# Optimization experiments

Hardware: AMD Instinct MI355X
Metric: run time of the kernel (lower is better)

The kernel has to match this reference:

```python
import jax, jax.numpy as jnp
import numpy as np

N = 100000
E = 3200000
IN_DIM, HID_DIM, OUT_DIM = 29, 64, 2


def setup_inputs() -> dict:
    key = jax.random.key(0)
    k1, k2, k3, k4, k5 = jax.random.split(key, 5)
    x = jax.random.normal(k1, (N, IN_DIM), dtype=jnp.float32)
    edge_index = jax.random.randint(k2, (2, E), 0, N, dtype=jnp.int64)
    # GCNConv params: glorot-ish weights, zero bias (bias added after aggregation)
    W1 = jax.random.normal(k3, (IN_DIM, HID_DIM), dtype=jnp.float32) * (1.0 / np.sqrt(IN_DIM))
    b1 = jnp.zeros((HID_DIM,), dtype=jnp.float32)
    W2 = jax.random.normal(k4, (HID_DIM, OUT_DIM), dtype=jnp.float32) * (1.0 / np.sqrt(HID_DIM))
    b2 = jnp.zeros((OUT_DIM,), dtype=jnp.float32)
    return {"x": x, "edge_index": edge_index, "W1": W1, "b1": b1, "W2": W2, "b2": b2}


def _gcn_norm(edge_index, n_nodes):
    # PyG gcn_norm with add_self_loops=True, symmetric D^-1/2 A D^-1/2
    loop = jnp.arange(n_nodes, dtype=edge_index.dtype)
    src = jnp.concatenate([edge_index[0], loop])
    dst = jnp.concatenate([edge_index[1], loop])
    deg = jax.ops.segment_sum(jnp.ones_like(dst, dtype=jnp.float32), dst, num_segments=n_nodes)
    dinv = jnp.where(deg > 0, jax.lax.rsqrt(deg), 0.0)
    norm = dinv[src] * dinv[dst]  # [E + N]
    return src, dst, norm


def _gcn_conv(x, src, dst, norm, W, b):
    h = x @ W                      # [N, d_out] -- transform first (smaller msgs)
    msg = h[src] * norm[:, None]   # [E+N, d_out] gather + scale
    out = jax.ops.segment_sum(msg, dst, num_segments=x.shape[0])  # scatter-add
    return out + b


def reference(x, edge_index, W1, b1, W2, b2):
    src, dst, norm = _gcn_norm(edge_index, x.shape[0])
    h = _gcn_conv(x, src, dst, norm, W1, b1)
    h = jax.nn.relu(h)
    out = _gcn_conv(h, src, dst, norm, W2, b2)
    return out
```

## Files before the change

### kernel.cpp

```cpp
#include <hip/hip_runtime.h>

#define N_NODES 100000
#define N_EDGES 3200000
#define IN_DIM  29
#define HID_DIM 64
#define NBUCK   391
#define BNODES  256
#define CAP     10496
#define PEPT    16
#define PEPB    16384
#define PSTAGE  22272

#define OFF_CUR   0
#define OFF_ROWS  512
#define OFF_ROWE  100512
#define OFF_DINV  200512
#define OFF_ZS    300512
#define OFF_EBUF  500544
#define OFF_XS    4604480

static __device__ __forceinline__ unsigned short f2bf(float f) {
    unsigned u = __float_as_uint(f);
    u += 0x7fffu + ((u >> 16) & 1u);
    return (unsigned short)(u >> 16);
}

static __device__ __forceinline__ void unpack_add(float4& acc, uint2 a) {
    acc.x += __uint_as_float(a.x << 16);
    acc.y += __uint_as_float(a.x & 0xFFFF0000u);
    acc.z += __uint_as_float(a.y << 16);
    acc.w += __uint_as_float(a.y & 0xFFFF0000u);
}

__global__ __launch_bounds__(1024) void partition_kernel(const int* __restrict__ ei,
        int* __restrict__ gcursor, int* __restrict__ ebuf) {
    __shared__ int lhist[NBUCK];
    __shared__ int lcur[NBUCK];
    __shared__ int gbase[NBUCK];
    __shared__ int soff[NBUCK];
    __shared__ int sc[NBUCK];
    __shared__ int stage[PSTAGE];
    int tid = threadIdx.x;
    for (int i = tid; i < NBUCK; i += 1024) lhist[i] = 0;
    __syncthreads();

    int base = blockIdx.x * PEPB + tid * PEPT;
    bool valid = (base < N_EDGES);
    if (valid) {
        const int4* dp = (const int4*)(ei + N_EDGES + base);
        #pragma unroll
        for (int q = 0; q < 4; ++q) {
            int4 t = dp[q];
            atomicAdd(&lhist[t.x >> 8], 1); atomicAdd(&lhist[t.y >> 8], 1);
            atomicAdd(&lhist[t.z >> 8], 1); atomicAdd(&lhist[t.w >> 8], 1);
        }
    }
    __syncthreads();
    int c = 0, p = 0;
    if (tid < NBUCK) { c = lhist[tid]; p = (c + 15) & ~15; sc[tid] = p; }
    __syncthreads();
    for (int off = 1; off < NBUCK; off <<= 1) {
        int t = 0;
        if (tid < NBUCK && tid >= off) t = sc[tid - off];
        __syncthreads();
        if (tid < NBUCK) sc[tid] += t;
        __syncthreads();
    }
    if (tid < NBUCK) {
        int so = sc[tid] - p;
        soff[tid] = so;
        lcur[tid] = so;
        gbase[tid] = p ? (tid * CAP + atomicAdd(&gcursor[tid], p)) : 0;
    }
    __syncthreads();
    if (valid) {
        const int4* dp = (const int4*)(ei + N_EDGES + base);
        const int4* sp = (const int4*)(ei + base);
        #pragma unroll
        for (int q = 0; q < 4; ++q) {
            int4 d = dp[q];
            int4 s = sp[q];
            int pos;
            pos = atomicAdd(&lcur[d.x >> 8], 1); stage[pos] = s.x | ((d.x & 255) << 17);
            pos = atomicAdd(&lcur[d.y >> 8], 1); stage[pos] = s.y | ((d.y & 255) << 17);
            pos = atomicAdd(&lcur[d.z >> 8], 1); stage[pos] = s.z | ((d.z & 255) << 17);
            pos = atomicAdd(&lcur[d.w >> 8], 1); stage[pos] = s.w | ((d.w & 255) << 17);
        }
    }
    __syncthreads();
    if (tid < NBUCK) {
        int endReal = lcur[tid];
        int endPad  = soff[tid] + (((lhist[tid]) + 15) & ~15);
        for (int k = endReal; k < endPad; ++k) stage[k] = -1;
    }
    __syncthreads();
    int wv = tid >> 6, ln = tid & 63;
    for (int b = wv; b < NBUCK; b += 16) {
        int np = (lhist[b] + 15) & ~15;
        int so = soff[b], gb = gbase[b];
        for (int k = ln; k < np; k += 64)
            ebuf[gb + k] = stage[so + k];
    }
}

__global__ __launch_bounds__(1024) void bucketsort_kernel(const int* __restrict__ gcursor,
        int* __restrict__ ebuf, int* __restrict__ rowStart, int* __restrict__ rowEnd,
        float* __restrict__ dinv, const float* __restrict__ x,
        unsigned int* __restrict__ xsb, float* __restrict__ zs) {
    __shared__ int   cnt[BNODES];
    __shared__ int   cur[BNODES];
    __shared__ float dls[BNODES];
    __shared__ int   stage[CAP];
    __shared__ int   szp_sh;
    int b = blockIdx.x, tid = threadIdx.x;
    if (tid < BNODES) cnt[tid] = 0;
    __syncthreads();
    int base = b * CAP;
    int size = gcursor[b];

    for (int j = tid; j < size; j += 1024) {
        unsigned p = (unsigned)ebuf[base + j];
        if (p != 0xFFFFFFFFu) atomicAdd(&cnt[p >> 17], 1);
    }
    __syncthreads();

    int v = 0, vp = 0;
    if (tid < BNODES) { v = cnt[tid]; vp = (v + 7) & ~7; cur[tid] = vp; }
    __syncthreads();
    for (int off = 1; off < BNODES; off <<= 1) {
        int t = 0;
        if (tid < BNODES && tid >= off) t = cur[tid - off];
        __syncthreads();
        if (tid < BNODES) cur[tid] += t;
        __syncthreads();
    }
    if (tid < BNODES) {
        int excl = cur[tid] - vp;
        int node = b * BNODES + tid;
        if (node < N_NODES) {
            rowStart[node] = base + excl;
            rowEnd[node]   = base + excl + vp;
            float dn = rsqrtf((float)v + 1.0f);
            dinv[node] = dn;
            dls[tid] = dn;
        }
        if (tid == BNODES - 1) szp_sh = cur[tid];
        cur[tid] = excl;
        for (int p2 = excl + v; p2 < excl + vp; ++p2)
            stage[p2] = N_NODES;
    }
    __syncthreads();

    for (int j = tid; j < size; j += 1024) {
        unsigned p = (unsigned)ebuf[base + j];
        if (p != 0xFFFFFFFFu) {
            int pos = atomicAdd(&cur[p >> 17], 1);
            stage[pos] = p & 0x1FFFF;
        }
    }
    __syncthreads();
    int szp = szp_sh;
    for (int j = tid; j < szp; j += 1024)
        ebuf[base + j] = stage[j];

    for (int i = tid; i < BNODES * 16; i += 1024) {
        int dl = i >> 4, kp = i & 15;
        int nd = b * BNODES + dl;
        if (nd < N_NODES) {
            float dn = dls[dl];
            int k0 = kp * 2, k1 = k0 + 1;
            float f0 = (k0 < IN_DIM) ? x[nd * IN_DIM + k0] * dn : 0.0f;
            float f1 = (k1 < IN_DIM) ? x[nd * IN_DIM + k1] * dn : 0.0f;
            xsb[(size_t)nd * 16 + kp] = (unsigned)f2bf(f0) | ((unsigned)f2bf(f1) << 16);
        } else if (nd == N_NODES) {
            xsb[(size_t)nd * 16 + kp] = 0u;
        }
    }
    if (b == 0 && tid == 0) {
        zs[2 * N_NODES]     = 0.0f;
        zs[2 * N_NODES + 1] = 0.0f;
    }
}

#define XROW(i) (((unsigned)(i) << 6) | moff)

#define PREP(P, rs, re, node)                                            \
    int P##i0, P##i1, P##i2, P##i3, P##i4, P##i5;                        \
    {                                                                    \
        int relim = max((re) - 1, (rs));                                 \
        int j0 = (rs) + q;                                               \
        int t0 = ebuf[min(j0,      relim)];                              \
        int t1 = ebuf[min(j0 + 8,  relim)];                              \
        int t2 = ebuf[min(j0 + 16, relim)];                              \
        int t3 = ebuf[min(j0 + 24, relim)];                              \
        int t4 = ebuf[min(j0 + 32, relim)];                              \
        P##i0 = (j0      < (re)) ? t0 : N_NODES;                         \
        P##i1 = (j0 + 8  < (re)) ? t1 : N_NODES;                         \
        P##i2 = (j0 + 16 < (re)) ? t2 : N_NODES;                         \
        P##i3 = (j0 + 24 < (re)) ? t3 : N_NODES;                         \
        P##i4 = (j0 + 32 < (re)) ? t4 : N_NODES;                         \
        P##i5 = (q == 0) ? (node) : N_NODES;    \
    }

#define GATH(G, P)                                                       \
    uint2 G##0 = *(const uint2*)(xb + XROW(P##i0));                      \
    uint2 G##1 = *(const uint2*)(xb + XROW(P##i1));                      \
    uint2 G##2 = *(const uint2*)(xb + XROW(P##i2));                      \
    uint2 G##3 = *(const uint2*)(xb + XROW(P##i3));                      \
    uint2 G##4 = *(const uint2*)(xb + XROW(P##i4));                      \
    uint2 G##5 = *(const uint2*)(xb + XROW(P##i5));

#define UNP(acc, G)                                                      \
    unpack_add(acc, G##0); unpack_add(acc, G##1); unpack_add(acc, G##2); \
    unpack_add(acc, G##3); unpack_add(acc, G##4); unpack_add(acc, G##5);

#define TAIL(acc, rs, re)                                                \
    {                                                                    \
        int j = (rs) + q + 40;                                           \
        while (j < (re)) {                  \
            int s = ebuf[j];                                             \
            uint2 a = *(const uint2*)(xb + XROW(s));                     \
            unpack_add(acc, a);                                          \
            j += 8;                                                      \
        }                                                                \
    }

static __device__ __forceinline__ void mlp2_store(float4 aA, float4 aB,
        int nodeA, int nodeB, int lane,
        const float* w1s, const float* b1s, const float* w2s,
        const float* __restrict__ dinv, float* __restrict__ zs) {
    #pragma unroll
    for (int msk = 8; msk <= 32; msk <<= 1) {
        aA.x += __shfl_xor(aA.x, msk); aB.x += __shfl_xor(aB.x, msk);
        aA.y += __shfl_xor(aA.y, msk); aB.y += __shfl_xor(aB.y, msk);
        aA.z += __shfl_xor(aA.z, msk); aB.z += __shfl_xor(aB.z, msk);
        aA.w += __shfl_xor(aA.w, msk); aB.w += __shfl_xor(aB.w, msk);
    }
    float dnA = dinv[nodeA], dnB = dinv[nodeB];
    aA.x *= dnA; aA.y *= dnA; aA.z *= dnA; aA.w *= dnA;
    aB.x *= dnB; aB.y *= dnB; aB.z *= dnB; aB.w *= dnB;

    float hA = b1s[lane], hB = b1s[lane];
    #pragma unroll
    for (int kk = 0; kk < IN_DIM; ++kk) {
        float w = w1s[kk * HID_DIM + lane];
        float cA = ((kk & 3) == 0) ? aA.x : ((kk & 3) == 1) ? aA.y
                 : ((kk & 3) == 2) ? aA.z : aA.w;
        float cB = ((kk & 3) == 0) ? aB.x : ((kk & 3) == 1) ? aB.y
                 : ((kk & 3) == 2) ? aB.z : aB.w;
        hA = fmaf(__shfl(cA, kk >> 2), w, hA);
        hB = fmaf(__shfl(cB, kk >> 2), w, hB);
    }
    hA = fmaxf(hA, 0.0f); hB = fmaxf(hB, 0.0f);

    float zA0 = hA * w2s[lane * 2 + 0], zA1 = hA * w2s[lane * 2 + 1];
    float zB0 = hB * w2s[lane * 2 + 0], zB1 = hB * w2s[lane * 2 + 1];
    #pragma unroll
    for (int off = 32; off > 0; off >>= 1) {
        zA0 += __shfl_down(zA0, off); zA1 += __shfl_down(zA1, off);
        zB0 += __shfl_down(zB0, off); zB1 += __shfl_down(zB1, off);
    }
    if (lane == 0) {
        float2 oA; oA.x = zA0 * dnA; oA.y = zA1 * dnA;
        float2 oB; oB.x = zB0 * dnB; oB.y = zB1 * dnB;
        *(float2*)(zs + nodeA * 2) = oA;
        *(float2*)(zs + nodeB * 2) = oB;
    }
}

__global__ __launch_bounds__(512, 4) void fused_kernel(const unsigned int* __restrict__ xs_,
        const int* __restrict__ rowStart, const int* __restrict__ rowEnd,
        const int* __restrict__ ebuf, const float* __restrict__ dinv,
        const float* __restrict__ W1, const float* __restrict__ b1,
        const float* __restrict__ W2, float* __restrict__ zs) {
    __shared__ float w1s[IN_DIM * HID_DIM];
    __shared__ float b1s[HID_DIM];
    __shared__ float w2s[HID_DIM * 2];
    const int tid = threadIdx.x;
    for (int i = tid; i < IN_DIM * HID_DIM; i += 512) w1s[i] = W1[i];
    if (tid < HID_DIM) {
        b1s[tid] = b1[tid];
        w2s[tid * 2 + 0] = W2[tid * 2 + 0];
        w2s[tid * 2 + 1] = W2[tid * 2 + 1];
    }
    __syncthreads();

    const int lane = tid & 63;
    const int q = lane >> 3, m = lane & 7;
    const unsigned moff = (unsigned)(m << 3);
    const char* xb = (const char*)xs_;
    const int n0 = blockIdx.x * 32 + (tid >> 6) * 4;

    const int rs0 = rowStart[n0+0], re0 = rowEnd[n0+0];
    const int rs1 = rowStart[n0+1], re1 = rowEnd[n0+1];
    const int rs2 = rowStart[n0+2], re2 = rowEnd[n0+2];
    const int rs3 = rowStart[n0+3], re3 = rowEnd[n0+3];

    PREP(pa, rs0, re0, n0+0)
    PREP(pb, rs1, re1, n0+1)
    PREP(pc, rs2, re2, n0+2)
    PREP(pd, rs3, re3, n0+3)
    GATH(ga, pa)
    GATH(gb, pb)
    GATH(gc, pc)
    GATH(gd, pd)

    float4 acc0 = make_float4(0.f, 0.f, 0.f, 0.f);
    float4 acc1 = make_float4(0.f, 0.f, 0.f, 0.f);
    float4 acc2 = make_float4(0.f, 0.f, 0.f, 0.f);
    float4 acc3 = make_float4(0.f, 0.f, 0.f, 0.f);
    UNP(acc0, ga)
    TAIL(acc0, rs0, re0)
    UNP(acc1, gb)
    TAIL(acc1, rs1, re1)
    UNP(acc2, gc)
    TAIL(acc2, rs2, re2)
    UNP(acc3, gd)
    TAIL(acc3, rs3, re3)
    mlp2_store(acc0, acc1, n0+0, n0+1, lane, w1s, b1s, w2s, dinv, zs);
    mlp2_store(acc2, acc3, n0+2, n0+3, lane, w1s, b1s, w2s, dinv, zs);
}

__global__ __launch_bounds__(256) void agg2_kernel(const float* __restrict__ zs,
        const int* __restrict__ rowStart, const int* __restrict__ rowEnd,
        const int* __restrict__ ebuf, const float* __restrict__ dinv,
        const float* __restrict__ b2, float* __restrict__ out) {
    int tid = threadIdx.x;
    int node = blockIdx.x * 16 + (tid >> 4);
    if (node >= N_NODES) return;
    int gl = tid & 15;
    const float2* zs2 = (const float2*)zs;
    float a0 = 0.0f, a1 = 0.0f, c0 = 0.0f, c1 = 0.0f;
    int rs = rowStart[node], re = rowEnd[node];
    int j = rs + gl;
    for (; j + 16 < re; j += 32) {
        float2 za = zs2[ebuf[j]];
        float2 zb = zs2[ebuf[j + 16]];
        a0 += za.x; a1 += za.y;
        c0 += zb.x; c1 += zb.y;
    }
    if (j < re) {
        float2 za = zs2[ebuf[j]];
        a0 += za.x; a1 += za.y;
    }
    a0 += c0; a1 += c1;
    a0 += __shfl_xor(a0, 8); a1 += __shfl_xor(a1, 8);
    a0 += __shfl_xor(a0, 4); a1 += __shfl_xor(a1, 4);
    a0 += __shfl_xor(a0, 2); a1 += __shfl_xor(a1, 2);
    a0 += __shfl_xor(a0, 1); a1 += __shfl_xor(a1, 1);
    if (gl == 0) {
        float dn = dinv[node];
        float2 zself = zs2[node];
        float2 o;
        o.x = dn * (a0 + zself.x) + b2[0];
        o.y = dn * (a1 + zself.y) + b2[1];
        ((float2*)out)[node] = o;
    }
}

extern "C" void kernel_launch(void* const* d_in, const int* in_sizes, int n_in,
                              void* d_out, int out_size, void* d_ws, size_t ws_size,
                              hipStream_t stream) {
    const float* x  = (const float*)d_in[0];
    const int*   ei = (const int*)d_in[1];
    const float* W1 = (const float*)d_in[2];
    const float* b1 = (const float*)d_in[3];
    const float* W2 = (const float*)d_in[4];
    const float* b2 = (const float*)d_in[5];
    float* out = (float*)d_out;

    int*   wsi      = (int*)d_ws;
    float* wsf      = (float*)d_ws;
    int*   gcursor  = wsi + OFF_CUR;
    int*   rowStart = wsi + OFF_ROWS;
    int*   rowEnd   = wsi + OFF_ROWE;
    float* dinv     = wsf + OFF_DINV;
    float* zs       = wsf + OFF_ZS;
    int*   ebuf     = wsi + OFF_EBUF;
    unsigned int* xsb = (unsigned int*)(wsi + OFF_XS);

    hipMemsetAsync(gcursor, 0, NBUCK * sizeof(int), stream);
    partition_kernel<<<(N_EDGES + PEPB - 1) / PEPB, 1024, 0, stream>>>(ei, gcursor, ebuf);
    bucketsort_kernel<<<NBUCK, 1024, 0, stream>>>(gcursor, ebuf, rowStart, rowEnd, dinv, x, xsb, zs);
    fused_kernel<<<N_NODES / 32, 512, 0, stream>>>(xsb, rowStart, rowEnd, ebuf, dinv, W1, b1, W2, zs);
    agg2_kernel<<<(N_NODES + 15) / 16, 256, 0, stream>>>(zs, rowStart, rowEnd, ebuf, dinv, b2, out);
}
```

Measured before the change: 201.5 us.

## Split layer-1 feature gather into two half-width passes over separate feature tables

The bf16 feature table is split into two 32-byte-per-node halves, and the layer-1 aggregation runs as two kernel passes, each gathering one half. The first pass writes partial sums to a workspace buffer, and the second pass combines them with its own half and runs the MLP. The aim is to make each pass's gather working set (3.2 MB instead of 6.4 MB) fit better in cache and to cut register pressure. In exchange, the edge index list is read twice, there is an extra launch, and partial sums make an extra round trip through memory. Gathers are also reordered to interleave with accumulation.

```diff
diff --git a/kernel.cpp b/kernel.cpp
--- a/kernel.cpp
+++ b/kernel.cpp
@@ -17,7 +17,9 @@
 #define OFF_DINV  200512
 #define OFF_ZS    300512
 #define OFF_EBUF  500544
-#define OFF_XS    4604480
+#define OFF_ACC   4604480
+#define OFF_XS0   6204480
+#define OFF_XS1   7004512
 
 static __device__ __forceinline__ unsigned short f2bf(float f) {
     unsigned u = __float_as_uint(f);
@@ -25,11 +27,9 @@
     return (unsigned short)(u >> 16);
 }
 
-static __device__ __forceinline__ void unpack_add(float4& acc, uint2 a) {
-    acc.x += __uint_as_float(a.x << 16);
-    acc.y += __uint_as_float(a.x & 0xFFFF0000u);
-    acc.z += __uint_as_float(a.y << 16);
-    acc.w += __uint_as_float(a.y & 0xFFFF0000u);
+static __device__ __forceinline__ void unpack_add2(float2& acc, unsigned a) {
+    acc.x += __uint_as_float(a << 16);
+    acc.y += __uint_as_float(a & 0xFFFF0000u);
 }
 
 __global__ __launch_bounds__(1024) void partition_kernel(const int* __restrict__ ei,
@@ -106,7 +106,8 @@
 __global__ __launch_bounds__(1024) void bucketsort_kernel(const int* __restrict__ gcursor,
         int* __restrict__ ebuf, int* __restrict__ rowStart, int* __restrict__ rowEnd,
         float* __restrict__ dinv, const float* __restrict__ x,
-        unsigned int* __restrict__ xsb, float* __restrict__ zs) {
+        unsigned int* __restrict__ xs0, unsigned int* __restrict__ xs1,
+        float* __restrict__ zs) {
     __shared__ int   cnt[BNODES];
     __shared__ int   cur[BNODES];
     __shared__ float dls[BNODES];
@@ -171,9 +172,12 @@
             int k0 = kp * 2, k1 = k0 + 1;
             float f0 = (k0 < IN_DIM) ? x[nd * IN_DIM + k0] * dn : 0.0f;
             float f1 = (k1 < IN_DIM) ? x[nd * IN_DIM + k1] * dn : 0.0f;
-            xsb[(size_t)nd * 16 + kp] = (unsigned)f2bf(f0) | ((unsigned)f2bf(f1) << 16);
+            unsigned u = (unsigned)f2bf(f0) | ((unsigned)f2bf(f1) << 16);
+            if (kp < 8) xs0[(size_t)nd * 8 + kp] = u;
+            else        xs1[(size_t)nd * 8 + (kp - 8)] = u;
         } else if (nd == N_NODES) {
-            xsb[(size_t)nd * 16 + kp] = 0u;
+            if (kp < 8) xs0[(size_t)nd * 8 + kp] = 0u;
+            else        xs1[(size_t)nd * 8 + (kp - 8)] = 0u;
         }
     }
     if (b == 0 && tid == 0) {
@@ -182,7 +186,7 @@
     }
 }
 
-#define XROW(i) (((unsigned)(i) << 6) | moff)
+#define XROWU(i) (((unsigned)(i) << 5) | moff)
 
 #define PREP(P, rs, re, node)                                            \
     int P##i0, P##i1, P##i2, P##i3, P##i4, P##i5;                        \
@@ -202,57 +206,52 @@
         P##i5 = (q == 0) ? (node) : N_NODES;    \
     }
 
-#define GATH(G, P)                                                       \
-    uint2 G##0 = *(const uint2*)(xb + XROW(P##i0));                      \
-    uint2 G##1 = *(const uint2*)(xb + XROW(P##i1));                      \
-    uint2 G##2 = *(const uint2*)(xb + XROW(P##i2));                      \
-    uint2 G##3 = *(const uint2*)(xb + XROW(P##i3));                      \
-    uint2 G##4 = *(const uint2*)(xb + XROW(P##i4));                      \
-    uint2 G##5 = *(const uint2*)(xb + XROW(P##i5));
-
-#define UNP(acc, G)                                                      \
-    unpack_add(acc, G##0); unpack_add(acc, G##1); unpack_add(acc, G##2); \
-    unpack_add(acc, G##3); unpack_add(acc, G##4); unpack_add(acc, G##5);
-
-#define TAIL(acc, rs, re)                                                \
+#define GATHU(G, P)                                                      \
+    unsigned G##0 = *(const unsigned*)(xb + XROWU(P##i0));               \
+    unsigned G##1 = *(const unsigned*)(xb + XROWU(P##i1));               \
+    unsigned G##2 = *(const unsigned*)(xb + XROWU(P##i2));               \
+    unsigned G##3 = *(const unsigned*)(xb + XROWU(P##i3));               \
+    unsigned G##4 = *(const unsigned*)(xb + XROWU(P##i4));               \
+    unsigned G##5 = *(const unsigned*)(xb + XROWU(P##i5));
+
+#define UNPU(acc, G)                                                     \
+    unpack_add2(acc, G##0); unpack_add2(acc, G##1); unpack_add2(acc, G##2); \
+    unpack_add2(acc, G##3); unpack_add2(acc, G##4); unpack_add2(acc, G##5);
+
+#define TAILU(acc, rs, re)                                               \
     {                                                                    \
         int j = (rs) + q + 40;                                           \
         while (j < (re)) {                  \
             int s = ebuf[j];                                             \
-            uint2 a = *(const uint2*)(xb + XROW(s));                     \
-            unpack_add(acc, a);                                          \
+            unsigned a = *(const unsigned*)(xb + XROWU(s));              \
+            unpack_add2(acc, a);                                         \
             j += 8;                                                      \
         }                                                                \
     }
 
-static __device__ __forceinline__ void mlp2_store(float4 aA, float4 aB,
-        int nodeA, int nodeB, int lane,
+#define FOLD2(acc)                                                       \
+    acc.x += __shfl_xor(acc.x, 8);  acc.y += __shfl_xor(acc.y, 8);       \
+    acc.x += __shfl_xor(acc.x, 16); acc.y += __shfl_xor(acc.y, 16);      \
+    acc.x += __shfl_xor(acc.x, 32); acc.y += __shfl_xor(acc.y, 32);
+
+static __device__ __forceinline__ void mlp2_fin(float4 aA, float4 aB,
+        int nodeA, int nodeB, int lane, float dnA, float dnB,
         const float* w1s, const float* b1s, const float* w2s,
-        const float* __restrict__ dinv, float* __restrict__ zs) {
-    #pragma unroll
-    for (int msk = 8; msk <= 32; msk <<= 1) {
-        aA.x += __shfl_xor(aA.x, msk); aB.x += __shfl_xor(aB.x, msk);
-        aA.y += __shfl_xor(aA.y, msk); aB.y += __shfl_xor(aB.y, msk);
-        aA.z += __shfl_xor(aA.z, msk); aB.z += __shfl_xor(aB.z, msk);
-        aA.w += __shfl_xor(aA.w, msk); aB.w += __shfl_xor(aB.w, msk);
-    }
-    float dnA = dinv[nodeA], dnB = dinv[nodeB];
+        float* __restrict__ zs) {
     aA.x *= dnA; aA.y *= dnA; aA.z *= dnA; aA.w *= dnA;
     aB.x *= dnB; aB.y *= dnB; aB.z *= dnB; aB.w *= dnB;
-
     float hA = b1s[lane], hB = b1s[lane];
     #pragma unroll
     for (int kk = 0; kk < IN_DIM; ++kk) {
         float w = w1s[kk * HID_DIM + lane];
-        float cA = ((kk & 3) == 0) ? aA.x : ((kk & 3) == 1) ? aA.y
-                 : ((kk & 3) == 2) ? aA.z : aA.w;
-        float cB = ((kk & 3) == 0) ? aB.x : ((kk & 3) == 1) ? aB.y
-                 : ((kk & 3) == 2) ? aB.z : aB.w;
-        hA = fmaf(__shfl(cA, kk >> 2), w, hA);
-        hB = fmaf(__shfl(cB, kk >> 2), w, hB);
+        float cA = (kk < 16) ? ((kk & 1) ? aA.y : aA.x)
+                             : ((kk & 1) ? aA.w : aA.z);
+        float cB = (kk < 16) ? ((kk & 1) ? aB.y : aB.x)
+                             : ((kk & 1) ? aB.w : aB.z);
+        hA = fmaf(__shfl(cA, (kk >> 1) & 7), w, hA);
+        hB = fmaf(__shfl(cB, (kk >> 1) & 7), w, hB);
     }
     hA = fmaxf(hA, 0.0f); hB = fmaxf(hB, 0.0f);
-
     float zA0 = hA * w2s[lane * 2 + 0], zA1 = hA * w2s[lane * 2 + 1];
     float zB0 = hB * w2s[lane * 2 + 0], zB1 = hB * w2s[lane * 2 + 1];
     #pragma unroll
@@ -268,26 +267,30 @@
     }
 }
 
-__global__ __launch_bounds__(512, 4) void fused_kernel(const unsigned int* __restrict__ xs_,
+template<int PHASE>
+__global__ __launch_bounds__(512) void fused_kernel(const unsigned int* __restrict__ xs_,
         const int* __restrict__ rowStart, const int* __restrict__ rowEnd,
         const int* __restrict__ ebuf, const float* __restrict__ dinv,
         const float* __restrict__ W1, const float* __restrict__ b1,
-        const float* __restrict__ W2, float* __restrict__ zs) {
+        const float* __restrict__ W2, float* __restrict__ accb,
+        float* __restrict__ zs) {
     __shared__ float w1s[IN_DIM * HID_DIM];
     __shared__ float b1s[HID_DIM];
     __shared__ float w2s[HID_DIM * 2];
     const int tid = threadIdx.x;
-    for (int i = tid; i < IN_DIM * HID_DIM; i += 512) w1s[i] = W1[i];
-    if (tid < HID_DIM) {
-        b1s[tid] = b1[tid];
-        w2s[tid * 2 + 0] = W2[tid * 2 + 0];
-        w2s[tid * 2 + 1] = W2[tid * 2 + 1];
-    }
-    __syncthreads();
+    if (PHASE == 1) {
+        for (int i = tid; i < IN_DIM * HID_DIM; i += 512) w1s[i] = W1[i];
+        if (tid < HID_DIM) {
+            b1s[tid] = b1[tid];
+            w2s[tid * 2 + 0] = W2[tid * 2 + 0];
+            w2s[tid * 2 + 1] = W2[tid * 2 + 1];
+        }
+        __syncthreads();
+    }
 
     const int lane = tid & 63;
     const int q = lane >> 3, m = lane & 7;
-    const unsigned moff = (unsigned)(m << 3);
+    const unsigned moff = (unsigned)(m << 2);
     const char* xb = (const char*)xs_;
     const int n0 = blockIdx.x * 32 + (tid >> 6) * 4;
 
@@ -298,27 +301,50 @@
 
     PREP(pa, rs0, re0, n0+0)
     PREP(pb, rs1, re1, n0+1)
+    GATHU(ga, pa)
+    GATHU(gb, pb)
     PREP(pc, rs2, re2, n0+2)
     PREP(pd, rs3, re3, n0+3)
-    GATH(ga, pa)
-    GATH(gb, pb)
-    GATH(gc, pc)
-    GATH(gd, pd)
-
-    float4 acc0 = make_float4(0.f, 0.f, 0.f, 0.f);
-    float4 acc1 = make_float4(0.f, 0.f, 0.f, 0.f);
-    float4 acc2 = make_float4(0.f, 0.f, 0.f, 0.f);
-    float4 acc3 = make_float4(0.f, 0.f, 0.f, 0.f);
-    UNP(acc0, ga)
-    TAIL(acc0, rs0, re0)
-    UNP(acc1, gb)
-    TAIL(acc1, rs1, re1)
-    UNP(acc2, gc)
-    TAIL(acc2, rs2, re2)
-    UNP(acc3, gd)
-    TAIL(acc3, rs3, re3)
-    mlp2_store(acc0, acc1, n0+0, n0+1, lane, w1s, b1s, w2s, dinv, zs);
-    mlp2_store(acc2, acc3, n0+2, n0+3, lane, w1s, b1s, w2s, dinv, zs);
+    float2 a0 = make_float2(0.f, 0.f), a1 = make_float2(0.f, 0.f);
+    UNPU(a0, ga)
+    TAILU(a0, rs0, re0)
+    UNPU(a1, gb)
+    TAILU(a1, rs1, re1)
+    GATHU(gc, pc)
+    GATHU(gd, pd)
+    FOLD2(a0)
+    FOLD2(a1)
+    float2 a2 = make_float2(0.f, 0.f), a3 = make_float2(0.f, 0.f);
+    UNPU(a2, gc)
+    TAILU(a2, rs2, re2)
+    UNPU(a3, gd)
+    TAILU(a3, rs3, re3)
+    FOLD2(a2)
+    FOLD2(a3)
+
+    if (PHASE == 0) {
+        if (q == 0) {
+            float2* ap = (float2*)accb;
+            ap[(n0+0) * 8 + m] = a0;
+            ap[(n0+1) * 8 + m] = a1;
+            ap[(n0+2) * 8 + m] = a2;
+            ap[(n0+3) * 8 + m] = a3;
+        }
+    } else {
+        const float2* ap = (const float2*)accb;
+        float2 h0a = ap[(n0+0) * 8 + m];
+        float2 h0b = ap[(n0+1) * 8 + m];
+        float2 h0c = ap[(n0+2) * 8 + m];
+        float2 h0d = ap[(n0+3) * 8 + m];
+        float dn0 = dinv[n0+0], dn1 = dinv[n0+1];
+        float dn2 = dinv[n0+2], dn3 = dinv[n0+3];
+        float4 A0; A0.x = h0a.x; A0.y = h0a.y; A0.z = a0.x; A0.w = a0.y;
+        float4 A1; A1.x = h0b.x; A1.y = h0b.y; A1.z = a1.x; A1.w = a1.y;
+        float4 A2; A2.x = h0c.x; A2.y = h0c.y; A2.z = a2.x; A2.w = a2.y;
+        float4 A3; A3.x = h0d.x; A3.y = h0d.y; A3.z = a3.x; A3.w = a3.y;
+        mlp2_fin(A0, A1, n0+0, n0+1, lane, dn0, dn1, w1s, b1s, w2s, zs);
+        mlp2_fin(A2, A3, n0+2, n0+3, lane, dn2, dn3, w1s, b1s, w2s, zs);
+    }
 }
 
 __global__ __launch_bounds__(256) void agg2_kernel(const float* __restrict__ zs,
@@ -377,11 +403,14 @@
     float* dinv     = wsf + OFF_DINV;
     float* zs       = wsf + OFF_ZS;
     int*   ebuf     = wsi + OFF_EBUF;
-    unsigned int* xsb = (unsigned int*)(wsi + OFF_XS);
+    float* accb     = wsf + OFF_ACC;
+    unsigned int* xs0 = (unsigned int*)(wsi + OFF_XS0);
+    unsigned int* xs1 = (unsigned int*)(wsi + OFF_XS1);
 
     hipMemsetAsync(gcursor, 0, NBUCK * sizeof(int), stream);
     partition_kernel<<<(N_EDGES + PEPB - 1) / PEPB, 1024, 0, stream>>>(ei, gcursor, ebuf);
-    bucketsort_kernel<<<NBUCK, 1024, 0, stream>>>(gcursor, ebuf, rowStart, rowEnd, dinv, x, xsb, zs);
-    fused_kernel<<<N_NODES / 32, 512, 0, stream>>>(xsb, rowStart, rowEnd, ebuf, dinv, W1, b1, W2, zs);
+    bucketsort_kernel<<<NBUCK, 1024, 0, stream>>>(gcursor, ebuf, rowStart, rowEnd, dinv, x, xs0, xs1, zs);
+    fused_kernel<0><<<N_NODES / 32, 512, 0, stream>>>(xs0, rowStart, rowEnd, ebuf, dinv, W1, b1, W2, accb, zs);
+    fused_kernel<1><<<N_NODES / 32, 512, 0, stream>>>(xs1, rowStart, rowEnd, ebuf, dinv, W1, b1, W2, accb, zs);
     agg2_kernel<<<(N_NODES + 15) / 16, 256, 0, stream>>>(zs, rowStart, rowEnd, ebuf, dinv, b2, out);
 }
```

Result: slower. 216.7 us (+7.6%).

## Widen fused gather to 16-byte loads with 16 edge lanes per node

Applied to the files above, without the earlier changes.

The first-layer aggregation now uses uint4 loads covering 8 bf16 features per lane, so 4 lanes cover a 64-byte row and 16 edges are processed in parallel per wavefront instead of 8. The self-loop gather moves out of the prepared batch and is added after the cross-lane fold. The gather/accumulate of the second node pair is interleaved with the first pair's processing. The occupancy hint in launch_bounds is dropped. Wider loads reduce instruction count per edge, while the changed interleaving and launch bounds may raise register pressure and lower occupancy.

```diff
diff --git a/kernel.cpp b/kernel.cpp
--- a/kernel.cpp
+++ b/kernel.cpp
@@ -25,11 +25,11 @@
     return (unsigned short)(u >> 16);
 }
 
-static __device__ __forceinline__ void unpack_add(float4& acc, uint2 a) {
-    acc.x += __uint_as_float(a.x << 16);
-    acc.y += __uint_as_float(a.x & 0xFFFF0000u);
-    acc.z += __uint_as_float(a.y << 16);
-    acc.w += __uint_as_float(a.y & 0xFFFF0000u);
+static __device__ __forceinline__ void upk8(float4& L, float4& H, uint4 a) {
+    L.x += __uint_as_float(a.x << 16); L.y += __uint_as_float(a.x & 0xFFFF0000u);
+    L.z += __uint_as_float(a.y << 16); L.w += __uint_as_float(a.y & 0xFFFF0000u);
+    H.x += __uint_as_float(a.z << 16); H.y += __uint_as_float(a.z & 0xFFFF0000u);
+    H.z += __uint_as_float(a.w << 16); H.w += __uint_as_float(a.w & 0xFFFF0000u);
 }
 
 __global__ __launch_bounds__(1024) void partition_kernel(const int* __restrict__ ei,
@@ -182,74 +182,74 @@
     }
 }
 
-#define XROW(i) (((unsigned)(i) << 6) | moff)
-
-#define PREP(P, rs, re, node)                                            \
-    int P##i0, P##i1, P##i2, P##i3, P##i4, P##i5;                        \
+#define XOFF(i) ((((unsigned)(i)) << 6) | (m << 4))
+
+#define PREP(P, rs, re)                                                  \
+    int P##i0, P##i1, P##i2;                                             \
     {                                                                    \
         int relim = max((re) - 1, (rs));                                 \
         int j0 = (rs) + q;                                               \
         int t0 = ebuf[min(j0,      relim)];                              \
-        int t1 = ebuf[min(j0 + 8,  relim)];                              \
-        int t2 = ebuf[min(j0 + 16, relim)];                              \
-        int t3 = ebuf[min(j0 + 24, relim)];                              \
-        int t4 = ebuf[min(j0 + 32, relim)];                              \
+        int t1 = ebuf[min(j0 + 16, relim)];                              \
+        int t2 = ebuf[min(j0 + 32, relim)];                              \
         P##i0 = (j0      < (re)) ? t0 : N_NODES;                         \
-        P##i1 = (j0 + 8  < (re)) ? t1 : N_NODES;                         \
-        P##i2 = (j0 + 16 < (re)) ? t2 : N_NODES;                         \
-        P##i3 = (j0 + 24 < (re)) ? t3 : N_NODES;                         \
-        P##i4 = (j0 + 32 < (re)) ? t4 : N_NODES;                         \
-        P##i5 = (q == 0) ? (node) : N_NODES;    \
-    }
-
-#define GATH(G, P)                                                       \
-    uint2 G##0 = *(const uint2*)(xb + XROW(P##i0));                      \
-    uint2 G##1 = *(const uint2*)(xb + XROW(P##i1));                      \
-    uint2 G##2 = *(const uint2*)(xb + XROW(P##i2));                      \
-    uint2 G##3 = *(const uint2*)(xb + XROW(P##i3));                      \
-    uint2 G##4 = *(const uint2*)(xb + XROW(P##i4));                      \
-    uint2 G##5 = *(const uint2*)(xb + XROW(P##i5));
-
-#define UNP(acc, G)                                                      \
-    unpack_add(acc, G##0); unpack_add(acc, G##1); unpack_add(acc, G##2); \
-    unpack_add(acc, G##3); unpack_add(acc, G##4); unpack_add(acc, G##5);
-
-#define TAIL(acc, rs, re)                                                \
-    {                                                                    \
-        int j = (rs) + q + 40;                                           \
+        P##i1 = (j0 + 16 < (re)) ? t1 : N_NODES;                         \
+        P##i2 = (j0 + 32 < (re)) ? t2 : N_NODES;                         \
+    }
+
+#define GATH(G, P)                                                      \
+    uint4 G##0 = *(const uint4*)(xb + XOFF(P##i0));                     \
+    uint4 G##1 = *(const uint4*)(xb + XOFF(P##i1));                     \
+    uint4 G##2 = *(const uint4*)(xb + XOFF(P##i2));
+
+#define UNP(L, H, G)                                                    \
+    upk8(L, H, G##0); upk8(L, H, G##1); upk8(L, H, G##2);
+
+#define TAIL(L, H, rs, re)                                              \
+    {                                                                   \
+        int j = (rs) + q + 48;                                          \
         while (j < (re)) {                  \
-            int s = ebuf[j];                                             \
-            uint2 a = *(const uint2*)(xb + XROW(s));                     \
-            unpack_add(acc, a);                                          \
-            j += 8;                                                      \
-        }                                                                \
-    }
-
-static __device__ __forceinline__ void mlp2_store(float4 aA, float4 aB,
+            int s = ebuf[j];                                            \
+            uint4 a = *(const uint4*)(xb + XOFF(s));                    \
+            upk8(L, H, a);                                              \
+            j += 16;                                                    \
+        }                                                               \
+    }
+
+static __device__ __forceinline__ void fold8(float4& L, float4& H) {
+    #pragma unroll
+    for (int msk = 4; msk <= 32; msk <<= 1) {
+        L.x += __shfl_xor(L.x, msk); L.y += __shfl_xor(L.y, msk);
+        L.z += __shfl_xor(L.z, msk); L.w += __shfl_xor(L.w, msk);
+        H.x += __shfl_xor(H.x, msk); H.y += __shfl_xor(H.y, msk);
+        H.z += __shfl_xor(H.z, msk); H.w += __shfl_xor(H.w, msk);
+    }
+}
+
+static __device__ __forceinline__ void mlp2_store(
+        float4 LA, float4 HA, float4 LB, float4 HB,
         int nodeA, int nodeB, int lane,
         const float* w1s, const float* b1s, const float* w2s,
         const float* __restrict__ dinv, float* __restrict__ zs) {
-    #pragma unroll
-    for (int msk = 8; msk <= 32; msk <<= 1) {
-        aA.x += __shfl_xor(aA.x, msk); aB.x += __shfl_xor(aB.x, msk);
-        aA.y += __shfl_xor(aA.y, msk); aB.y += __shfl_xor(aB.y, msk);
-        aA.z += __shfl_xor(aA.z, msk); aB.z += __shfl_xor(aB.z, msk);
-        aA.w += __shfl_xor(aA.w, msk); aB.w += __shfl_xor(aB.w, msk);
-    }
     float dnA = dinv[nodeA], dnB = dinv[nodeB];
-    aA.x *= dnA; aA.y *= dnA; aA.z *= dnA; aA.w *= dnA;
-    aB.x *= dnB; aB.y *= dnB; aB.z *= dnB; aB.w *= dnB;
+    LA.x *= dnA; LA.y *= dnA; LA.z *= dnA; LA.w *= dnA;
+    HA.x *= dnA; HA.y *= dnA; HA.z *= dnA; HA.w *= dnA;
+    LB.x *= dnB; LB.y *= dnB; LB.z *= dnB; LB.w *= dnB;
+    HB.x *= dnB; HB.y *= dnB; HB.z *= dnB; HB.w *= dnB;
 
     float hA = b1s[lane], hB = b1s[lane];
     #pragma unroll
     for (int kk = 0; kk < IN_DIM; ++kk) {
         float w = w1s[kk * HID_DIM + lane];
-        float cA = ((kk & 3) == 0) ? aA.x : ((kk & 3) == 1) ? aA.y
-                 : ((kk & 3) == 2) ? aA.z : aA.w;
-        float cB = ((kk & 3) == 0) ? aB.x : ((kk & 3) == 1) ? aB.y
-                 : ((kk & 3) == 2) ? aB.z : aB.w;
-        hA = fmaf(__shfl(cA, kk >> 2), w, hA);
-        hB = fmaf(__shfl(cB, kk >> 2), w, hB);
+        int r = kk & 7;
+        float cA = (r == 0) ? LA.x : (r == 1) ? LA.y : (r == 2) ? LA.z
+                 : (r == 3) ? LA.w : (r == 4) ? HA.x : (r == 5) ? HA.y
+                 : (r == 6) ? HA.z : HA.w;
+        float cB = (r == 0) ? LB.x : (r == 1) ? LB.y : (r == 2) ? LB.z
+                 : (r == 3) ? LB.w : (r == 4) ? HB.x : (r == 5) ? HB.y
+                 : (r == 6) ? HB.z : HB.w;
+        hA = fmaf(__shfl(cA, kk >> 3), w, hA);
+        hB = fmaf(__shfl(cB, kk >> 3), w, hB);
     }
     hA = fmaxf(hA, 0.0f); hB = fmaxf(hB, 0.0f);
 
@@ -268,7 +268,7 @@
     }
 }
 
-__global__ __launch_bounds__(512, 4) void fused_kernel(const unsigned int* __restrict__ xs_,
+__global__ __launch_bounds__(512) void fused_kernel(const unsigned int* __restrict__ xs_,
         const int* __restrict__ rowStart, const int* __restrict__ rowEnd,
         const int* __restrict__ ebuf, const float* __restrict__ dinv,
         const float* __restrict__ W1, const float* __restrict__ b1,
@@ -286,8 +286,8 @@
     __syncthreads();
 
     const int lane = tid & 63;
-    const int q = lane >> 3, m = lane & 7;
-    const unsigned moff = (unsigned)(m << 3);
+    const int q = lane >> 2;
+    const int m = lane & 3;
     const char* xb = (const char*)xs_;
     const int n0 = blockIdx.x * 32 + (tid >> 6) * 4;
 
@@ -296,29 +296,39 @@
     const int rs2 = rowStart[n0+2], re2 = rowEnd[n0+2];
     const int rs3 = rowStart[n0+3], re3 = rowEnd[n0+3];
 
-    PREP(pa, rs0, re0, n0+0)
-    PREP(pb, rs1, re1, n0+1)
-    PREP(pc, rs2, re2, n0+2)
-    PREP(pd, rs3, re3, n0+3)
+    PREP(pa, rs0, re0)
+    PREP(pb, rs1, re1)
     GATH(ga, pa)
     GATH(gb, pb)
+    PREP(pc, rs2, re2)
+    PREP(pd, rs3, re3)
+    float4 LA = {0,0,0,0}, HA = {0,0,0,0}, LB = {0,0,0,0}, HB = {0,0,0,0};
+    UNP(LA, HA, ga)
+    TAIL(LA, HA, rs0, re0)
+    UNP(LB, HB, gb)
+    TAIL(LB, HB, rs1, re1)
     GATH(gc, pc)
     GATH(gd, pd)
-
-    float4 acc0 = make_float4(0.f, 0.f, 0.f, 0.f);
-    float4 acc1 = make_float4(0.f, 0.f, 0.f, 0.f);
-    float4 acc2 = make_float4(0.f, 0.f, 0.f, 0.f);
-    float4 acc3 = make_float4(0.f, 0.f, 0.f, 0.f);
-    UNP(acc0, ga)
-    TAIL(acc0, rs0, re0)
-    UNP(acc1, gb)
-    TAIL(acc1, rs1, re1)
-    UNP(acc2, gc)
-    TAIL(acc2, rs2, re2)
-    UNP(acc3, gd)
-    TAIL(acc3, rs3, re3)
-    mlp2_store(acc0, acc1, n0+0, n0+1, lane, w1s, b1s, w2s, dinv, zs);
-    mlp2_store(acc2, acc3, n0+2, n0+3, lane, w1s, b1s, w2s, dinv, zs);
+    uint4 svA = *(const uint4*)(xb + XOFF(n0+0));
+    uint4 svB = *(const uint4*)(xb + XOFF(n0+1));
+    fold8(LA, HA);
+    fold8(LB, HB);
+    upk8(LA, HA, svA);
+    upk8(LB, HB, svB);
+    mlp2_store(LA, HA, LB, HB, n0+0, n0+1, lane, w1s, b1s, w2s, dinv, zs);
+
+    float4 LC = {0,0,0,0}, HC = {0,0,0,0}, LD = {0,0,0,0}, HD = {0,0,0,0};
+    UNP(LC, HC, gc)
+    TAIL(LC, HC, rs2, re2)
+    UNP(LD, HD, gd)
+    TAIL(LD, HD, rs3, re3)
+    uint4 svC = *(const uint4*)(xb + XOFF(n0+2));
+    uint4 svD = *(const uint4*)(xb + XOFF(n0+3));
+    fold8(LC, HC);
+    fold8(LD, HD);
+    upk8(LC, HC, svC);
+    upk8(LD, HD, svD);
+    mlp2_store(LC, HC, LD, HD, n0+2, n0+3, lane, w1s, b1s, w2s, dinv, zs);
 }
 
 __global__ __launch_bounds__(256) void agg2_kernel(const float* __restrict__ zs,
```

Measured after the change: 224.4 us. 1.11x slower.
